# Kernel optimization log

Measured on AMD Instinct MI355X. Metric: run time of the kernel, lower is better.

The kernel has to match this reference:

```python
import jax, jax.numpy as jnp
import numpy as np

HEADS = 16
HEAD_DIM = 64
DIM = 1024
INNER = HEADS * HEAD_DIM
EPS = 1e-5


def setup_inputs() -> dict:
    key = jax.random.key(0)
    ks = jax.random.split(key, 7)
    s_qkv = (2.0 / (DIM + 3 * INNER)) ** 0.5
    s_out = (2.0 / (INNER + DIM)) ** 0.5
    return {
        "x": jax.random.normal(ks[0], (4, 2048, DIM), dtype=jnp.float32),
        "w_qkv": jax.random.normal(ks[1], (DIM, 3 * INNER), dtype=jnp.float32) * s_qkv,
        "b_qkv": jnp.zeros((3 * INNER,), dtype=jnp.float32),
        "w_out": jax.random.normal(ks[2], (INNER, DIM), dtype=jnp.float32) * s_out,
        "b_out": jnp.zeros((DIM,), dtype=jnp.float32),
        "ln_gamma": jnp.ones((DIM,), dtype=jnp.float32),
        "ln_beta": jnp.zeros((DIM,), dtype=jnp.float32),
    }


def reference(x, w_qkv, b_qkv, w_out, b_out, ln_gamma, ln_beta):
    # Pre-norm LayerNorm
    mu = jnp.mean(x, axis=-1, keepdims=True)
    var = jnp.var(x, axis=-1, keepdims=True)
    xn = (x - mu) * jax.lax.rsqrt(var + EPS) * ln_gamma + ln_beta
    # QKV projection: [b, l, 3*inner]
    qkv = xn @ w_qkv + b_qkv
    q, k, v = jnp.split(qkv, 3, axis=-1)
    b, l, _ = x.shape
    def heads(t):  # [b, l, inner] -> [b, h, l, d]
        return t.reshape(b, l, HEADS, HEAD_DIM).transpose(0, 2, 1, 3)
    q, k, v = heads(q), heads(k), heads(v)
    scale = HEAD_DIM ** -0.5
    scores = jnp.einsum('bhqd,bhkd->bhqk', q, k) * scale
    att = jax.nn.softmax(scores, axis=-1)
    out = jnp.einsum('bhqk,bhkd->bhqd', att, v)
    out = out.transpose(0, 2, 1, 3).reshape(b, l, INNER)
    return out @ w_out + b_out
```

## Files before the change

### kernel.cpp

```cpp
#include <hip/hip_runtime.h>
#include <stdint.h>

typedef __bf16 bf16;
typedef bf16 bf16x4 __attribute__((ext_vector_type(4)));
typedef bf16 bf16x8 __attribute__((ext_vector_type(8)));
typedef float f32x4 __attribute__((ext_vector_type(4)));


__device__ __forceinline__ void gll16(const bf16* g, const bf16* l) {
  __builtin_amdgcn_global_load_lds(
      (__attribute__((address_space(1))) void*)(g),
      (__attribute__((address_space(3))) void*)(l),
      16, 0, 0);
}

__global__ __launch_bounds__(256) void ln_kernel(
    const float* __restrict__ x, const float* __restrict__ gamma,
    const float* __restrict__ beta, bf16* __restrict__ xn)
{
  __shared__ float red[8];
  const long row = blockIdx.x;
  const int t = threadIdx.x;
  f32x4 f = *(const f32x4*)(x + row * 1024 + t * 4);
  float sum = f[0] + f[1] + f[2] + f[3];
  float sq  = f[0]*f[0] + f[1]*f[1] + f[2]*f[2] + f[3]*f[3];
#pragma unroll
  for (int sh = 1; sh < 64; sh <<= 1) {
    sum += __shfl_xor(sum, sh, 64);
    sq  += __shfl_xor(sq,  sh, 64);
  }
  const int wave = t >> 6, lane = t & 63;
  if (lane == 0) { red[wave] = sum; red[wave + 4] = sq; }
  __syncthreads();
  sum = red[0] + red[1] + red[2] + red[3];
  sq  = red[4] + red[5] + red[6] + red[7];
  const float mu  = sum * (1.0f / 1024.0f);
  const float var = sq * (1.0f / 1024.0f) - mu * mu;
  const float rs  = rsqrtf(var + 1e-5f);
  f32x4 g = *(const f32x4*)(gamma + t * 4);
  f32x4 bb = *(const f32x4*)(beta + t * 4);
  bf16x4 ov;
#pragma unroll
  for (int i = 0; i < 4; i++)
    ov[i] = (bf16)((f[i] - mu) * rs * g[i] + bb[i]);
  *(bf16x4*)(xn + row * 1024 + t * 4) = ov;
}

__global__ __launch_bounds__(256) void transpose_kernel(
    const float* __restrict__ in, bf16* __restrict__ out, int R, int Cc)
{
  __shared__ bf16 tile[32][33];
  const int c0 = blockIdx.x * 32, r0 = blockIdx.y * 32;
  const int tx = threadIdx.x & 31, ty = threadIdx.x >> 5;
#pragma unroll
  for (int i = 0; i < 32; i += 8)
    tile[ty + i][tx] = (bf16)in[(long)(r0 + ty + i) * Cc + c0 + tx];
  __syncthreads();
#pragma unroll
  for (int i = 0; i < 32; i += 8)
    out[(long)(c0 + ty + i) * R + r0 + tx] = tile[tx][ty + i];
}

__global__ __launch_bounds__(256, 2) void gemm_bt(
    const bf16* __restrict__ A, const bf16* __restrict__ BT,
    const float* __restrict__ bias, float* __restrict__ C,
    bf16* __restrict__ qb, bf16* __restrict__ kb, bf16* __restrict__ vtb,
    int K, int N, int mode)
{
  __shared__ bf16 sA[128 * 32];
  __shared__ bf16 sB[128 * 32];
  const int t = threadIdx.x;
  const int lane = t & 63;
  const int wave = t >> 6;
  const int wave_u = __builtin_amdgcn_readfirstlane(wave);
  const int quad = lane >> 4;
  const int c16 = lane & 15;
  const int wm = (wave >> 1) * 64;
  const int wn = (wave & 1) * 64;
  const int m0 = blockIdx.x * 128;
  const int n0 = blockIdx.y * 128;

  f32x4 acc[4][4] = {};

  const int srow = t >> 2;
  const int scol = (t & 3) * 8;
  const bf16* gA = A + (long)(m0 + srow) * K + scol;
  const bf16* gB = BT + (long)(n0 + srow) * K + scol;
  const bf16* lA = sA + wave_u * 512;
  const bf16* lB = sB + wave_u * 512;
  const long rowskip = (long)64 * K;

  for (int k0 = 0; k0 < K; k0 += 32) {
    gll16(gA + k0, lA);
    gll16(gA + k0 + rowskip, lA + 2048);
    gll16(gB + k0, lB);
    gll16(gB + k0 + rowskip, lB + 2048);
    __syncthreads();
    bf16x8 af[4], bfr[4];
#pragma unroll
    for (int i = 0; i < 4; i++)
      af[i] = *(const bf16x8*)(sA + (wm + i * 16 + c16) * 32 + quad * 8);
#pragma unroll
    for (int j = 0; j < 4; j++)
      bfr[j] = *(const bf16x8*)(sB + (wn + j * 16 + c16) * 32 + quad * 8);
#pragma unroll
    for (int i = 0; i < 4; i++)
#pragma unroll
      for (int j = 0; j < 4; j++)
        acc[i][j] = __builtin_amdgcn_mfma_f32_16x16x32_bf16(af[i], bfr[j], acc[i][j], 0, 0, 0);
    __syncthreads();
  }

#pragma unroll
  for (int i = 0; i < 4; i++) {
    const int mbase = m0 + wm + i * 16 + quad * 4;
#pragma unroll
    for (int j = 0; j < 4; j++) {
      const int n = n0 + wn + j * 16 + c16;
      const float bv = bias[n];
      if (mode == 0) {
#pragma unroll
        for (int r = 0; r < 4; r++)
          C[(long)(mbase + r) * N + n] = acc[i][j][r] + bv;
      } else {
        const int part = n >> 10;
        const int inner = n & 1023;
        const int h = inner >> 6, d = inner & 63;
#pragma unroll
        for (int r = 0; r < 4; r++) {
          const int m = mbase + r;
          const int b = m >> 11, l = m & 2047;
          const long bh = (long)((b << 4) | h);
          const float v = acc[i][j][r] + bv;
          if (part == 0)      qb [(bh * 2048 + l) * 64 + d] = (bf16)(v * 0.18033688f);
          else if (part == 1) kb [(bh * 2048 + l) * 64 + d] = (bf16)v;
          else                vtb[(bh * 64 + d) * 2048 + l] = (bf16)v;
        }
      }
    }
  }
}

__global__ __launch_bounds__(256, 4) void attn_kernel(
    const bf16* __restrict__ q, const bf16* __restrict__ k,
    const bf16* __restrict__ vt, bf16* __restrict__ att)
{
  __shared__ bf16 sK[128 * 68];
  __shared__ bf16 sVt[64 * 132];

  const int i = blockIdx.x;
  const int xcd = i & 7;
  const int wi = i >> 3;
  const int qt = wi & 15;
  const int bh = xcd * 8 + (wi >> 4);
  const int b = bh >> 4, h = bh & 15;
  const int q0 = qt * 128;
  const int t = threadIdx.x;
  const int wave = t >> 6, lane = t & 63;
  const int quad = lane >> 4, c16 = lane & 15;

  const bf16* qp = q + (long)bh * (2048 * 64);
  const bf16* kp = k + (long)bh * (2048 * 64);
  const bf16* vp = vt + (long)bh * (64 * 2048);

  bf16x8 aq[2][2];
#pragma unroll
  for (int m = 0; m < 2; m++) {
    const bf16* qrow = qp + (long)(q0 + wave * 32 + m * 16 + c16) * 64 + quad * 8;
    aq[m][0] = *(const bf16x8*)(qrow);
    aq[m][1] = *(const bf16x8*)(qrow + 32);
  }

  float p_sum[2] = {0.0f, 0.0f};
  f32x4 o_acc[2][4] = {};

  const int kr = t >> 3;
  const int kd = (t & 7) * 8;
  const int vr = t >> 4;
  const int vc = t & 15;
  const int vl = vc * 8;
  const int vD0 = (vc >> 2) * 32 + (vc & 1) * 16 + ((vc >> 1) & 1) * 4;

  bf16x8 kreg[4], vreg[4];
#pragma unroll
  for (int it = 0; it < 4; it++) {
    kreg[it] = *(const bf16x8*)(kp + (long)(it * 32 + kr) * 64 + kd);
    vreg[it] = *(const bf16x8*)(vp + (long)(it * 16 + vr) * 2048 + vl);
  }

  for (int kt = 0; kt < 16; kt++) {
    __syncthreads();
#pragma unroll
    for (int it = 0; it < 4; it++)
      *(bf16x8*)&sK[(it * 32 + kr) * 68 + kd] = kreg[it];
#pragma unroll
    for (int it = 0; it < 4; it++) {
      const bf16x8 v = vreg[it];
      const bf16x4 lo = __builtin_shufflevector(v, v, 0, 1, 2, 3);
      const bf16x4 hi = __builtin_shufflevector(v, v, 4, 5, 6, 7);
      bf16* d = &sVt[(it * 16 + vr) * 132 + vD0];
      *(bf16x4*)(d)     = lo;
      *(bf16x4*)(d + 8) = hi;
    }
    __syncthreads();

    const int kvn = ((kt + 1) & 15) * 128;

#pragma unroll
    for (int ks = 0; ks < 4; ks++) {
      bf16x8 ap[2];
#pragma unroll
      for (int e = 0; e < 2; e++) {
        const int jb = ks * 2 + e;
        const bf16x8 bk0 = *(const bf16x8*)&sK[(jb * 16 + c16) * 68 + quad * 8];
        const bf16x8 bk1 = *(const bf16x8*)&sK[(jb * 16 + c16) * 68 + 32 + quad * 8];
#pragma unroll
        for (int m = 0; m < 2; m++) {
          f32x4 z = {};
          z = __builtin_amdgcn_mfma_f32_16x16x32_bf16(bk0, aq[m][0], z, 0, 0, 0);
          z = __builtin_amdgcn_mfma_f32_16x16x32_bf16(bk1, aq[m][1], z, 0, 0, 0);
#pragma unroll
          for (int r = 0; r < 4; r++) {
            const float p = __builtin_amdgcn_exp2f(z[r]);
            p_sum[m] += p;
            ap[m][e * 4 + r] = (bf16)p;
          }
        }
      }
      if (ks == 1) {
#pragma unroll
        for (int it = 0; it < 4; it++)
          kreg[it] = *(const bf16x8*)(kp + (long)(kvn + it * 32 + kr) * 64 + kd);
      }
      if (ks == 2) {
#pragma unroll
        for (int it = 0; it < 4; it++)
          vreg[it] = *(const bf16x8*)(vp + (long)(it * 16 + vr) * 2048 + kvn + vl);
      }
#pragma unroll
      for (int jd = 0; jd < 4; jd++) {
        const bf16x8 bv = *(const bf16x8*)&sVt[(jd * 16 + c16) * 132 + ks * 32 + quad * 8];
        o_acc[0][jd] = __builtin_amdgcn_mfma_f32_16x16x32_bf16(ap[0], bv, o_acc[0][jd], 0, 0, 0);
        o_acc[1][jd] = __builtin_amdgcn_mfma_f32_16x16x32_bf16(ap[1], bv, o_acc[1][jd], 0, 0, 0);
      }
    }
  }

#pragma unroll
  for (int m = 0; m < 2; m++) {
    p_sum[m] += __shfl_xor(p_sum[m], 16, 64);
    p_sum[m] += __shfl_xor(p_sum[m], 32, 64);
  }

#pragma unroll
  for (int m = 0; m < 2; m++) {
#pragma unroll
    for (int r = 0; r < 4; r++) {
      const float ps = __shfl(p_sum[m], quad * 4 + r, 64);
      const float inv = 1.0f / ps;
      const long rowbase = ((long)b * 2048 + q0 + wave * 32 + m * 16 + quad * 4 + r) * 1024 + h * 64;
#pragma unroll
      for (int jd = 0; jd < 4; jd++)
        att[rowbase + jd * 16 + c16] = (bf16)(o_acc[m][jd][r] * inv);
    }
  }
}

extern "C" void kernel_launch(void* const* d_in, const int* in_sizes, int n_in,
                              void* d_out, int out_size, void* d_ws, size_t ws_size,
                              hipStream_t stream) {
  (void)in_sizes; (void)n_in; (void)out_size; (void)ws_size;
  const float* x     = (const float*)d_in[0];
  const float* w_qkv = (const float*)d_in[1];
  const float* b_qkv = (const float*)d_in[2];
  const float* w_out = (const float*)d_in[3];
  const float* b_out = (const float*)d_in[4];
  const float* gamma = (const float*)d_in[5];
  const float* beta  = (const float*)d_in[6];
  float* out = (float*)d_out;
  bf16* ws  = (bf16*)d_ws;

  bf16* xn    = ws;
  bf16* wqkvT = ws + 8388608;
  bf16* woutT = wqkvT + 3145728;
  bf16* qbuf  = woutT + 1048576;
  bf16* kbuf  = qbuf + 8388608;
  bf16* vtbuf = kbuf + 8388608;
  bf16* att   = xn;

  transpose_kernel<<<dim3(3072 / 32, 1024 / 32), 256, 0, stream>>>(w_qkv, wqkvT, 1024, 3072);
  transpose_kernel<<<dim3(1024 / 32, 1024 / 32), 256, 0, stream>>>(w_out, woutT, 1024, 1024);
  ln_kernel<<<dim3(8192), 256, 0, stream>>>(x, gamma, beta, xn);
  gemm_bt<<<dim3(8192 / 128, 3072 / 128), 256, 0, stream>>>(
      xn, wqkvT, b_qkv, (float*)nullptr, qbuf, kbuf, vtbuf, 1024, 3072, 1);
  attn_kernel<<<dim3(1024), 256, 0, stream>>>(qbuf, kbuf, vtbuf, att);
  gemm_bt<<<dim3(8192 / 128, 1024 / 128), 256, 0, stream>>>(
      att, woutT, b_out, out, (bf16*)nullptr, (bf16*)nullptr, (bf16*)nullptr, 1024, 1024, 0);
}
```

Baseline: 296.8 us.

## Double-buffer GEMM LDS tiles and merge weight transposes into one launch

The bf16 GEMM now keeps two LDS buffers for the A and B tiles. It issues the global-to-LDS loads for the next K step right after the barrier, then runs MFMAs on the current buffer, which removes one __syncthreads per iteration and overlaps memory with compute. The two weight transpose launches are folded into a single grid that picks its source matrix from the block index, saving one launch. LDS use per block doubles, and correctness depends on the barrier waiting for the outstanding global_load_lds transfers.

```diff
diff --git a/kernel.cpp b/kernel.cpp
--- a/kernel.cpp
+++ b/kernel.cpp
@@ -46,11 +46,18 @@
   *(bf16x4*)(xn + row * 1024 + t * 4) = ov;
 }
 
-__global__ __launch_bounds__(256) void transpose_kernel(
-    const float* __restrict__ in, bf16* __restrict__ out, int R, int Cc)
+__global__ __launch_bounds__(256) void transpose2_kernel(
+    const float* __restrict__ wqkv, bf16* __restrict__ wqkvT,
+    const float* __restrict__ wout, bf16* __restrict__ woutT)
 {
   __shared__ bf16 tile[32][33];
-  const int c0 = blockIdx.x * 32, r0 = blockIdx.y * 32;
+  const int bx = blockIdx.x;
+  const float* in;
+  bf16* out;
+  int Cc, c0;
+  if (bx < 96) { in = wqkv; out = wqkvT; Cc = 3072; c0 = bx * 32; }
+  else         { in = wout; out = woutT; Cc = 1024; c0 = (bx - 96) * 32; }
+  const int r0 = blockIdx.y * 32;
   const int tx = threadIdx.x & 31, ty = threadIdx.x >> 5;
 #pragma unroll
   for (int i = 0; i < 32; i += 8)
@@ -58,7 +65,7 @@
   __syncthreads();
 #pragma unroll
   for (int i = 0; i < 32; i += 8)
-    out[(long)(c0 + ty + i) * R + r0 + tx] = tile[tx][ty + i];
+    out[(long)(c0 + ty + i) * 1024 + r0 + tx] = tile[tx][ty + i];
 }
 
 __global__ __launch_bounds__(256, 2) void gemm_bt(
@@ -67,8 +74,8 @@
     bf16* __restrict__ qb, bf16* __restrict__ kb, bf16* __restrict__ vtb,
     int K, int N, int mode)
 {
-  __shared__ bf16 sA[128 * 32];
-  __shared__ bf16 sB[128 * 32];
+  __shared__ bf16 sA[2][128 * 32];
+  __shared__ bf16 sB[2][128 * 32];
   const int t = threadIdx.x;
   const int lane = t & 63;
   const int wave = t >> 6;
@@ -86,29 +93,41 @@
   const int scol = (t & 3) * 8;
   const bf16* gA = A + (long)(m0 + srow) * K + scol;
   const bf16* gB = BT + (long)(n0 + srow) * K + scol;
-  const bf16* lA = sA + wave_u * 512;
-  const bf16* lB = sB + wave_u * 512;
+  const bf16* lA = sA[0] + wave_u * 512;
+  const bf16* lB = sB[0] + wave_u * 512;
   const long rowskip = (long)64 * K;
 
+  gll16(gA, lA);
+  gll16(gA + rowskip, lA + 2048);
+  gll16(gB, lB);
+  gll16(gB + rowskip, lB + 2048);
+
+  int cur = 0;
   for (int k0 = 0; k0 < K; k0 += 32) {
-    gll16(gA + k0, lA);
-    gll16(gA + k0 + rowskip, lA + 2048);
-    gll16(gB + k0, lB);
-    gll16(gB + k0 + rowskip, lB + 2048);
     __syncthreads();
+    const int kn = k0 + 32;
+    if (kn < K) {
+      const int alt = cur ^ 1;
+      gll16(gA + kn, lA + alt * 4096);
+      gll16(gA + kn + rowskip, lA + alt * 4096 + 2048);
+      gll16(gB + kn, lB + alt * 4096);
+      gll16(gB + kn + rowskip, lB + alt * 4096 + 2048);
+    }
+    const bf16* cA = sA[0] + cur * 4096;
+    const bf16* cB = sB[0] + cur * 4096;
     bf16x8 af[4], bfr[4];
 #pragma unroll
     for (int i = 0; i < 4; i++)
-      af[i] = *(const bf16x8*)(sA + (wm + i * 16 + c16) * 32 + quad * 8);
+      af[i] = *(const bf16x8*)(cA + (wm + i * 16 + c16) * 32 + quad * 8);
 #pragma unroll
     for (int j = 0; j < 4; j++)
-      bfr[j] = *(const bf16x8*)(sB + (wn + j * 16 + c16) * 32 + quad * 8);
+      bfr[j] = *(const bf16x8*)(cB + (wn + j * 16 + c16) * 32 + quad * 8);
 #pragma unroll
     for (int i = 0; i < 4; i++)
 #pragma unroll
       for (int j = 0; j < 4; j++)
         acc[i][j] = __builtin_amdgcn_mfma_f32_16x16x32_bf16(af[i], bfr[j], acc[i][j], 0, 0, 0);
-    __syncthreads();
+    cur ^= 1;
   }
 
 #pragma unroll
@@ -288,8 +307,7 @@
   bf16* vtbuf = kbuf + 8388608;
   bf16* att   = xn;
 
-  transpose_kernel<<<dim3(3072 / 32, 1024 / 32), 256, 0, stream>>>(w_qkv, wqkvT, 1024, 3072);
-  transpose_kernel<<<dim3(1024 / 32, 1024 / 32), 256, 0, stream>>>(w_out, woutT, 1024, 1024);
+  transpose2_kernel<<<dim3(128, 32), 256, 0, stream>>>(w_qkv, wqkvT, w_out, woutT);
   ln_kernel<<<dim3(8192), 256, 0, stream>>>(x, gamma, beta, xn);
   gemm_bt<<<dim3(8192 / 128, 3072 / 128), 256, 0, stream>>>(
       xn, wqkvT, b_qkv, (float*)nullptr, qbuf, kbuf, vtbuf, 1024, 3072, 1);
```

New measurement: 279.4 us. -5.9%, faster.
